# Kernel tuning notes

Measured on AMD Instinct MI355X. Metric: run time of the kernel, lower is better.

## Reference

```python
import jax, jax.numpy as jnp
import numpy as np

B, T, C = 2, 2048, 2048
N_HEAD = 16
HS = C // N_HEAD
D_LATENT = C // 2


def setup_inputs() -> dict:
    key = jax.random.key(0)
    ks = jax.random.split(key, 7)
    s = 0.02
    return {
        "x": jax.random.normal(ks[0], (B, T, C), dtype=jnp.float32),
        "Wq": jax.random.normal(ks[1], (C, C), dtype=jnp.float32) * s,
        "Wc": jax.random.normal(ks[2], (C, D_LATENT), dtype=jnp.float32) * s,
        "Wk": jax.random.normal(ks[3], (D_LATENT, C), dtype=jnp.float32) * s,
        "Wv": jax.random.normal(ks[4], (D_LATENT, C), dtype=jnp.float32) * s,
        "Wo": jax.random.normal(ks[5], (C, C), dtype=jnp.float32) * s,
        "bo": jnp.zeros((C,), dtype=jnp.float32),
    }


def reference(x, Wq, Wc, Wk, Wv, Wo, bo):
    b, t, c = x.shape
    # projections (torch Linear without bias, weights stored as (in, out))
    q = x @ Wq                    # (B,T,C)
    c_latent = x @ Wc             # (B,T,d_latent)
    k = c_latent @ Wk             # (B,T,C)
    v = c_latent @ Wv             # (B,T,C)
    # split heads -> (B,H,T,hs)
    q = q.reshape(b, t, N_HEAD, HS).transpose(0, 2, 1, 3)
    k = k.reshape(b, t, N_HEAD, HS).transpose(0, 2, 1, 3)
    v = v.reshape(b, t, N_HEAD, HS).transpose(0, 2, 1, 3)
    scale = 1.0 / jnp.sqrt(jnp.asarray(HS, dtype=x.dtype))
    scores = jnp.einsum('bhqd,bhkd->bhqk', q, k) * scale
    causal = jnp.tril(jnp.ones((t, t), dtype=bool))
    scores = jnp.where(causal, scores, jnp.finfo(scores.dtype).min)
    attn = jax.nn.softmax(scores, axis=-1)
    y = jnp.einsum('bhqk,bhkd->bhqd', attn, v)      # (B,H,T,hs)
    y = y.transpose(0, 2, 1, 3).reshape(b, t, c)
    return y @ Wo + bo
```

## Files before the change

### kernel.cpp

```cpp
#include <hip/hip_runtime.h>
#include <hip/hip_bf16.h>
#include <math.h>

typedef __hip_bfloat16 bf16;
typedef __attribute__((ext_vector_type(8))) short bf16x8;
typedef __attribute__((ext_vector_type(4))) float f32x4;

#define B_  2
#define T_  2048
#define C_  2048
#define H_  16
#define HS_ 128
#define DL_ 1024
#define M_  (B_ * T_)
#define NT64_ 32

__device__ inline void lds16(const bf16* g, bf16* l) {
    __builtin_amdgcn_global_load_lds(
        (const __attribute__((address_space(1))) void*)g,
        (__attribute__((address_space(3))) void*)l, 16, 0, 0);
}

__global__ __launch_bounds__(256) void cast_bf16_k(
    const float* __restrict__ in, bf16* __restrict__ out)
{
    const size_t i = ((size_t)blockIdx.x * 256 + threadIdx.x) * 8;
    const float4 a = *(const float4*)(in + i);
    const float4 b = *(const float4*)(in + i + 4);
    bf16 o[8];
    o[0] = __float2bfloat16(a.x); o[1] = __float2bfloat16(a.y);
    o[2] = __float2bfloat16(a.z); o[3] = __float2bfloat16(a.w);
    o[4] = __float2bfloat16(b.x); o[5] = __float2bfloat16(b.y);
    o[6] = __float2bfloat16(b.z); o[7] = __float2bfloat16(b.w);
    *(uint4*)(out + i) = *(const uint4*)o;
}

__global__ __launch_bounds__(256) void transpose_cast5(
    const float* __restrict__ s0, const float* __restrict__ s1,
    const float* __restrict__ s2, const float* __restrict__ s3,
    const float* __restrict__ s4,
    bf16* __restrict__ d0, bf16* __restrict__ d1, bf16* __restrict__ d2,
    bf16* __restrict__ d3, bf16* __restrict__ d4)
{
    const float* in; bf16* out; int R, Cc;
    switch (blockIdx.z) {
        case 0: in = s0; out = d0; R = C_;  Cc = C_;  break;
        case 1: in = s1; out = d1; R = C_;  Cc = DL_; break;
        case 2: in = s2; out = d2; R = DL_; Cc = C_;  break;
        case 3: in = s3; out = d3; R = DL_; Cc = C_;  break;
        default: in = s4; out = d4; R = C_; Cc = C_;  break;
    }
    const int bx = blockIdx.x * 32, by = blockIdx.y * 32;
    if (bx >= Cc || by >= R) return;
    __shared__ float t[32][33];
    const int tx = threadIdx.x & 31, ty = threadIdx.x >> 5;
#pragma unroll
    for (int i = 0; i < 32; i += 8)
        t[ty + i][tx] = in[(size_t)(by + ty + i) * Cc + bx + tx];
    __syncthreads();
#pragma unroll
    for (int i = 0; i < 32; i += 8)
        out[(size_t)(bx + ty + i) * R + by + tx] = __float2bfloat16(t[tx][ty + i]);
}

#define GEMM250_CORE(A_, Bt_, ldA_, ldB_, Kdim_)                               \
    __shared__ __align__(16) bf16 smem[3 * 24576];                 \
    const int tid  = threadIdx.x;                                              \
    const int lane = tid & 63;                                                 \
    const int wid  = tid >> 6;                                       \
    const int wr   = wid >> 1, wc = wid & 1;                    \
    const int quad = lane >> 4, l16 = lane & 15;                               \
    const int sw8  = (l16 >> 1) & 7;                                           \
    f32x4 acc[4][4];                                                           \
    _Pragma("unroll")                                                          \
    for (int i = 0; i < 4; i++)                                                \
        _Pragma("unroll")                                                      \
        for (int j = 0; j < 4; j++) acc[i][j] = (f32x4){0.f, 0.f, 0.f, 0.f};   \
    const int sr  = tid >> 3;                                       \
    const int ssl = ((tid & 7) ^ ((sr >> 1) & 7)) * 8;                         \
    const bf16* pa = (A_)  + (size_t)(m0 + sr) * (ldA_) + ssl;                 \
    const bf16* pb = (Bt_) + (size_t)(n0 + sr) * (ldB_) + ssl;                 \
    const size_t a64 = (size_t)64 * (ldA_), b64 = (size_t)64 * (ldB_);         \
    const int NT = (Kdim_) / 64;                                               \
    _Pragma("unroll")                                                          \
    for (int pt = 0; pt < 2; ++pt) {                  \
        bf16* dst = smem + pt * 24576 + tid * 8;                               \
        const size_t ko = (size_t)pt * 64;                                     \
        lds16(pa + ko,           dst);                                         \
        lds16(pa + a64 + ko,     dst + 4096);                                  \
        lds16(pa + 2*a64 + ko,   dst + 8192);                                  \
        lds16(pa + 3*a64 + ko,   dst + 12288);                                 \
        lds16(pb + ko,           dst + 16384);                                 \
        lds16(pb + b64 + ko,     dst + 20480);                                 \
    }                                                                          \
    int cur = 0, nxt2 = 2;                                                     \
    for (int t = 0; t < NT; ++t) {                                             \
        if (t == NT - 1) {                                                     \
            __asm__ __volatile__("s_waitcnt vmcnt(0)" ::: "memory");           \
        } else {                                                               \
            __asm__ __volatile__("s_waitcnt vmcnt(6)" ::: "memory");           \
        }                                                                      \
        __builtin_amdgcn_s_barrier();                                          \
        __builtin_amdgcn_sched_barrier(0);                                     \
        if (t + 2 < NT) {                                                      \
            bf16* dst = smem + nxt2 * 24576 + tid * 8;                         \
            const size_t ko = (size_t)(t + 2) * 64;                            \
            lds16(pa + ko,           dst);                                     \
            lds16(pa + a64 + ko,     dst + 4096);                              \
            lds16(pa + 2*a64 + ko,   dst + 8192);                              \
            lds16(pa + 3*a64 + ko,   dst + 12288);                             \
            lds16(pb + ko,           dst + 16384);                             \
            lds16(pb + b64 + ko,     dst + 20480);                             \
        }                                                                      \
        const bf16* Ab = smem + cur * 24576;                                   \
        const bf16* Bb = Ab + 16384;                                           \
        bf16x8 af[4][2], bfr[4][2];                                            \
        _Pragma("unroll")                                                      \
        for (int mi = 0; mi < 4; mi++)                                         \
            _Pragma("unroll")                                                  \
            for (int ks = 0; ks < 2; ks++)                                     \
                af[mi][ks] = *(const bf16x8*)&Ab[(wr*64 + mi*16 + l16)*64 +    \
                                                 (((ks<<2)|quad) ^ sw8)*8];    \
        _Pragma("unroll")                                                      \
        for (int ni = 0; ni < 4; ni++)                                         \
            _Pragma("unroll")                                                  \
            for (int ks = 0; ks < 2; ks++)                                     \
                bfr[ni][ks] = *(const bf16x8*)&Bb[(wc*64 + ni*16 + l16)*64 +   \
                                                  (((ks<<2)|quad) ^ sw8)*8];   \
        __builtin_amdgcn_s_setprio(1);                                         \
        _Pragma("unroll")                                                      \
        for (int ks = 0; ks < 2; ks++)                                         \
            _Pragma("unroll")                                                  \
            for (int mi = 0; mi < 4; mi++)                                     \
                _Pragma("unroll")                                              \
                for (int ni = 0; ni < 4; ni++)                                 \
                    acc[mi][ni] = __builtin_amdgcn_mfma_f32_16x16x32_bf16(     \
                        af[mi][ks], bfr[ni][ks], acc[mi][ni], 0, 0, 0);        \
        __builtin_amdgcn_s_setprio(0);                                         \
        cur  = (cur  == 2) ? 0 : cur  + 1;                                     \
        nxt2 = (nxt2 == 2) ? 0 : nxt2 + 1;                                     \
    }

__global__ __launch_bounds__(512, 2) void gemm_qc_250(
    const bf16* __restrict__ A, const bf16* __restrict__ Bt,
    bf16* __restrict__ Cq, bf16* __restrict__ Cc)
{
    const int m0 = blockIdx.y * 256, n0 = blockIdx.x * 128;
    GEMM250_CORE(A, Bt, C_, C_, C_)
    const bool is_q = (n0 < C_);
    const float scl = is_q ? 0.08838834764831845f : 1.0f;
    bf16* dst = is_q ? Cq : Cc;
    const int ld   = is_q ? C_ : DL_;
    const int coff = is_q ? 0 : C_;
#pragma unroll
    for (int mi = 0; mi < 4; mi++) {
#pragma unroll
        for (int ni = 0; ni < 4; ni++) {
            const int col = n0 - coff + wc * 64 + ni * 16 + l16;
#pragma unroll
            for (int r = 0; r < 4; r++) {
                const int row = m0 + wr * 64 + mi * 16 + quad * 4 + r;
                dst[(size_t)row * ld + col] = __float2bfloat16(acc[mi][ni][r] * scl);
            }
        }
    }
}

__global__ __launch_bounds__(512, 2) void gemm_kv_250(
    const bf16* __restrict__ clat, const bf16* __restrict__ Wk_t,
    const bf16* __restrict__ Wv_t, bf16* __restrict__ kk, bf16* __restrict__ vt)
{
    const int bid = blockIdx.x;
    const bf16 *A, *Bt; bf16* dst; int N, m0, n0;
    if (bid < 256) { A = clat; Bt = Wk_t; dst = kk; N = C_;
                     m0 = (bid >> 4) * 256; n0 = (bid & 15) * 128; }
    else           { const int t2 = bid - 256;
                     A = Wv_t; Bt = clat; dst = vt; N = M_;
                     m0 = (t2 >> 5) * 256; n0 = (t2 & 31) * 128; }
    GEMM250_CORE(A, Bt, DL_, DL_, DL_)
#pragma unroll
    for (int mi = 0; mi < 4; mi++) {
#pragma unroll
        for (int ni = 0; ni < 4; ni++) {
            const int col = n0 + wc * 64 + ni * 16 + l16;
#pragma unroll
            for (int r = 0; r < 4; r++) {
                const int row = m0 + wr * 64 + mi * 16 + quad * 4 + r;
                dst[(size_t)row * N + col] = __float2bfloat16(acc[mi][ni][r]);
            }
        }
    }
}

__global__ __launch_bounds__(512, 2) void gemm_out_250(
    const bf16* __restrict__ A, const bf16* __restrict__ Bt,
    float* __restrict__ Cf32, const float* __restrict__ bias)
{
    const int m0 = blockIdx.y * 256, n0 = blockIdx.x * 128;
    GEMM250_CORE(A, Bt, C_, C_, C_)
#pragma unroll
    for (int mi = 0; mi < 4; mi++) {
#pragma unroll
        for (int ni = 0; ni < 4; ni++) {
            const int col = n0 + wc * 64 + ni * 16 + l16;
#pragma unroll
            for (int r = 0; r < 4; r++) {
                const int row = m0 + wr * 64 + mi * 16 + quad * 4 + r;
                Cf32[(size_t)row * C_ + col] = acc[mi][ni][r] + bias[col];
            }
        }
    }
}

__global__ __launch_bounds__(256, 3) void flash_sb(
    const bf16* __restrict__ Q, const bf16* __restrict__ K,
    const bf16* __restrict__ Vt, bf16* __restrict__ Y)
{
    __shared__ __align__(16) bf16 Ks[4][64][32];
    __shared__ __align__(16) bf16 Vs[2][128][32];
    __shared__ __align__(16) bf16 Ps[4][16][72];
    const int tid  = threadIdx.x;
    const int lane = tid & 63, wv = tid >> 6;
    const int quad = lane >> 4, l16 = lane & 15;
    const int sw = (l16 >> 1) & 3;
    const int bid = blockIdx.x;
    const int bh = (bid & 7) * 4 + ((bid >> 3) & 3);
    const int pa = (NT64_ - 1) - (bid >> 5);
    const int b = bh >> 4, h = bh & 15;
    const int q0 = pa * 64;
    const int nj = pa + 1;
    const int rb = q0 + wv * 16;

    const int sr  = tid >> 2;
    const int ssl = ((tid & 3) ^ ((sr >> 1) & 3)) * 8;

    bf16x8 qf[4];
    {
        const size_t rQ = (size_t)(b * T_ + q0 + wv * 16 + l16) * C_ + h * HS_;
#pragma unroll
        for (int c = 0; c < 4; c++)
            qf[c] = *(const bf16x8*)(Q + rQ + c * 32 + quad * 8);
    }

    f32x4 o[8];
#pragma unroll
    for (int dt = 0; dt < 8; dt++) o[dt] = (f32x4){0.f, 0.f, 0.f, 0.f};
    float l_s[4] = {0.f, 0.f, 0.f, 0.f};

    auto stageK = [&](int j) {
        const int kv0 = j * 64;
#pragma unroll
        for (int kc = 0; kc < 4; kc++)
            lds16(K + (size_t)(b * T_ + kv0 + sr) * C_ + h * HS_ + kc * 32 + ssl,
                  &Ks[kc][0][0] + tid * 8);
    };
    auto stageV = [&](int j) {
        const int kv0 = j * 64;
#pragma unroll
        for (int vc = 0; vc < 2; vc++)
#pragma unroll
            for (int hf = 0; hf < 2; hf++)
                lds16(Vt + (size_t)(h * HS_ + hf * 64 + sr) * M_ + b * T_ + kv0 + vc * 32 + ssl,
                      &Vs[vc][hf * 64][0] + tid * 8);
    };

    auto sm_half = [&](const f32x4* s, int nt0, bool diag, int kv0) {
        float p[2][4];
#pragma unroll
        for (int t = 0; t < 2; t++)
#pragma unroll
            for (int r = 0; r < 4; r++) {
                const int nt = nt0 + t;
                float e = __expf(s[nt][r]);
                if (diag) {
                    const int col = kv0 + nt * 16 + l16;
                    const int row = rb + quad * 4 + r;
                    if (col > row) e = 0.f;
                }
                p[t][r] = e;
            }
#pragma unroll
        for (int r = 0; r < 4; r++) l_s[r] += p[0][r] + p[1][r];
#pragma unroll
        for (int t = 0; t < 2; t++)
#pragma unroll
            for (int r = 0; r < 4; r++)
                Ps[wv][quad * 4 + r][(nt0 + t) * 16 + l16] = __float2bfloat16(p[t][r]);
        return *(const bf16x8*)&Ps[wv][l16][nt0 * 16 + quad * 8];
    };

    stageK(0);
    stageV(0);
    for (int j = 0; j < nj; j++) {
        const int kv0 = j * 64;
        const bool more = (j + 1 < nj);

        __asm__ __volatile__("s_waitcnt vmcnt(4)" ::: "memory");
        __builtin_amdgcn_s_barrier();
        __builtin_amdgcn_sched_barrier(0);

        f32x4 s[4];
#pragma unroll
        for (int nt = 0; nt < 4; nt++) s[nt] = (f32x4){0.f, 0.f, 0.f, 0.f};
        __builtin_amdgcn_s_setprio(1);
#pragma unroll
        for (int c = 0; c < 4; c++) {
            bf16x8 kf[4];
#pragma unroll
            for (int nt = 0; nt < 4; nt++)
                kf[nt] = *(const bf16x8*)&Ks[c][nt * 16 + l16][(quad ^ sw) * 8];
#pragma unroll
            for (int nt = 0; nt < 4; nt++)
                s[nt] = __builtin_amdgcn_mfma_f32_16x16x32_bf16(qf[c], kf[nt], s[nt], 0, 0, 0);
        }
        __builtin_amdgcn_s_setprio(0);

        __asm__ __volatile__("s_waitcnt lgkmcnt(0)" ::: "memory");
        __builtin_amdgcn_s_barrier();
        __builtin_amdgcn_sched_barrier(0);
        if (more) stageK(j + 1);

        const bool dg = (j == nj - 1);
        const bf16x8 p0 = sm_half(s, 0, dg, kv0);
        const bf16x8 p1 = sm_half(s, 2, dg, kv0);

        if (more) {
            __asm__ __volatile__("s_waitcnt vmcnt(4)" ::: "memory");
        } else {
            __asm__ __volatile__("s_waitcnt vmcnt(0)" ::: "memory");
        }
        __builtin_amdgcn_s_barrier();
        __builtin_amdgcn_sched_barrier(0);

        __builtin_amdgcn_s_setprio(1);
#pragma unroll
        for (int dt = 0; dt < 8; dt++) {
            const bf16x8 vf0 = *(const bf16x8*)&Vs[0][dt * 16 + l16][(quad ^ sw) * 8];
            o[dt] = __builtin_amdgcn_mfma_f32_16x16x32_bf16(p0, vf0, o[dt], 0, 0, 0);
        }
#pragma unroll
        for (int dt = 0; dt < 8; dt++) {
            const bf16x8 vf1 = *(const bf16x8*)&Vs[1][dt * 16 + l16][(quad ^ sw) * 8];
            o[dt] = __builtin_amdgcn_mfma_f32_16x16x32_bf16(p1, vf1, o[dt], 0, 0, 0);
        }
        __builtin_amdgcn_s_setprio(0);

        __asm__ __volatile__("s_waitcnt lgkmcnt(0)" ::: "memory");
        __builtin_amdgcn_s_barrier();
        __builtin_amdgcn_sched_barrier(0);
        if (more) stageV(j + 1);
    }

    {
        float inv[4];
#pragma unroll
        for (int r = 0; r < 4; r++) {
            float l = l_s[r];
            l += __shfl_xor(l, 1);
            l += __shfl_xor(l, 2);
            l += __shfl_xor(l, 4);
            l += __shfl_xor(l, 8);
            inv[r] = 1.f / l;
        }
#pragma unroll
        for (int dt = 0; dt < 8; dt++)
#pragma unroll
            for (int r = 0; r < 4; r++)
                Y[(size_t)(b * T_ + rb + quad * 4 + r) * C_ + h * HS_ + dt * 16 + l16] =
                    __float2bfloat16(o[dt][r] * inv[r]);
    }
}

extern "C" void kernel_launch(void* const* d_in, const int* in_sizes, int n_in,
                              void* d_out, int out_size, void* d_ws, size_t ws_size,
                              hipStream_t stream) {
    const float* x  = (const float*)d_in[0];
    const float* Wq = (const float*)d_in[1];
    const float* Wc = (const float*)d_in[2];
    const float* Wk = (const float*)d_in[3];
    const float* Wv = (const float*)d_in[4];
    const float* Wo = (const float*)d_in[5];
    const float* bo = (const float*)d_in[6];
    float* out = (float*)d_out;

    bf16* ws   = (bf16*)d_ws;
    bf16* x_bf = ws;
    bf16* Wq_t = x_bf + (size_t)M_ * C_;
    bf16* Wc_t = Wq_t + (size_t)C_ * C_;
    bf16* Wk_t = Wc_t + (size_t)DL_ * C_;
    bf16* Wv_t = Wk_t + (size_t)C_ * DL_;
    bf16* Wo_t = Wv_t + (size_t)C_ * DL_;
    bf16* q    = Wo_t + (size_t)C_ * C_;
    bf16* clat = q    + (size_t)M_ * C_;
    bf16* kk   = clat + (size_t)M_ * DL_;
    bf16* vt   = kk   + (size_t)M_ * C_;
    bf16* y    = vt   + (size_t)C_ * M_;

    const dim3 blk(256);
    const dim3 blk512(512);

    cast_bf16_k<<<dim3((M_ * C_) / (256 * 8)), blk, 0, stream>>>(x, x_bf);
    transpose_cast5<<<dim3(C_ / 32, C_ / 32, 5), blk, 0, stream>>>(
        Wq, Wc, Wk, Wv, Wo, Wq_t, Wc_t, Wk_t, Wv_t, Wo_t);

    gemm_qc_250<<<dim3((C_ + DL_) / 128, M_ / 256), blk512, 0, stream>>>(
        x_bf, Wq_t, q, clat);
    gemm_kv_250<<<dim3(512), blk512, 0, stream>>>(clat, Wk_t, Wv_t, kk, vt);

    flash_sb<<<dim3(NT64_ * H_ * B_), blk, 0, stream>>>(q, kk, vt, y);

    gemm_out_250<<<dim3(C_ / 128, M_ / 256), blk512, 0, stream>>>(
        y, Wo_t, out, bo);
}
```

Before: 329.1 us.

## Replace QC and KV GEMMs with 256x256 tile ping-pong kernel using phased MFMA

```diff
diff --git a/kernel.cpp b/kernel.cpp
--- a/kernel.cpp
+++ b/kernel.cpp
@@ -61,6 +61,150 @@
 #pragma unroll
     for (int i = 0; i < 32; i += 8)
         out[(size_t)(bx + ty + i) * R + by + tx] = __float2bfloat16(t[tx][ty + i]);
+}
+
+#define STAGE_AQ(qq, ko, bb)                                                   \
+    lds16(pa + (size_t)(qq) * 64 * (size_t)ldA + (ko),                         \
+          &As[bb][0][0] + (qq) * 4096 + tid * 8);
+#define STAGE_BQ(qq, ko, bb)                                                   \
+    lds16(pb + (size_t)(qq) * 64 * (size_t)ldB + (ko),                         \
+          &Bs[bb][0][0] + (qq) * 4096 + tid * 8);
+
+#define PHASE8(qm_, qn_)                                                       \
+    {                                                                          \
+        bf16x8 af[4][2], bfr[2][2];                                            \
+        _Pragma("unroll")                                                      \
+        for (int mi = 0; mi < 4; mi++)                                         \
+            _Pragma("unroll")                                                  \
+            for (int ks = 0; ks < 2; ks++)                                     \
+                af[mi][ks] = *(const bf16x8*)&Abase[((qm_)*64 + mi*16 + l16)*64\
+                                     + (((ks<<2)|quad) ^ sw8)*8];              \
+        _Pragma("unroll")                                                      \
+        for (int ni = 0; ni < 2; ni++)                                         \
+            _Pragma("unroll")                                                  \
+            for (int ks = 0; ks < 2; ks++)                                     \
+                bfr[ni][ks] = *(const bf16x8*)&Bbase[((qn_)*32 + ni*16 + l16)*64\
+                                     + (((ks<<2)|quad) ^ sw8)*8];              \
+        __builtin_amdgcn_s_barrier();                                          \
+        __asm__ __volatile__("s_waitcnt lgkmcnt(0)" ::: "memory");             \
+        __builtin_amdgcn_sched_barrier(0);                                     \
+        __builtin_amdgcn_s_setprio(1);                                         \
+        _Pragma("unroll")                                                      \
+        for (int ks = 0; ks < 2; ks++)                                         \
+            _Pragma("unroll")                                                  \
+            for (int mi = 0; mi < 4; mi++)                                     \
+                _Pragma("unroll")                                              \
+                for (int ni = 0; ni < 2; ni++)                                 \
+                    acc[(qm_)*4 + mi][(qn_)*2 + ni] =                          \
+                        __builtin_amdgcn_mfma_f32_16x16x32_bf16(               \
+                            af[mi][ks], bfr[ni][ks],                           \
+                            acc[(qm_)*4 + mi][(qn_)*2 + ni], 0, 0, 0);         \
+        __builtin_amdgcn_s_setprio(0);                                         \
+        __builtin_amdgcn_s_barrier();                                          \
+    }
+
+#define GEMM8P_CORE(A_, Bt_, ldA_, ldB_, Kdim_)                                \
+    __shared__ __align__(16) bf16 As[2][256][64];                   \
+    __shared__ __align__(16) bf16 Bs[2][256][64];                   \
+    const int tid  = threadIdx.x;                                              \
+    const int lane = tid & 63;                                                 \
+    const int wid  = tid >> 6;                                       \
+    const int wm   = wid >> 2, wn = wid & 3;                      \
+    const int quad = lane >> 4, l16 = lane & 15;                               \
+    const int sw8  = (l16 >> 1) & 7;                                           \
+    const int ldA = (ldA_), ldB = (ldB_);                                      \
+    f32x4 acc[8][4];                                                           \
+    _Pragma("unroll")                                                          \
+    for (int i = 0; i < 8; i++)                                                \
+        _Pragma("unroll")                                                      \
+        for (int j = 0; j < 4; j++) acc[i][j] = (f32x4){0.f, 0.f, 0.f, 0.f};   \
+    const int sr  = tid >> 3;                            \
+    const int ssl = ((tid & 7) ^ ((sr >> 1) & 7)) * 8;                         \
+    const bf16* pa = (A_)  + (size_t)(m0 + sr) * ldA + ssl;                    \
+    const bf16* pb = (Bt_) + (size_t)(n0 + sr) * ldB + ssl;                    \
+    const int NT = (Kdim_) / 64;                                               \
+    _Pragma("unroll")                                                          \
+    for (int pt = 0; pt < 2; ++pt) {                  \
+        const size_t ko = (size_t)pt * 64;                                     \
+        STAGE_AQ(0, ko, pt) STAGE_AQ(1, ko, pt)                                \
+        STAGE_AQ(2, ko, pt) STAGE_AQ(3, ko, pt)                                \
+        STAGE_BQ(0, ko, pt) STAGE_BQ(1, ko, pt)                                \
+        STAGE_BQ(2, ko, pt) STAGE_BQ(3, ko, pt)                                \
+    }                                                                          \
+    for (int t = 0; t < NT; ++t) {                                             \
+        const int buf = t & 1;                                                 \
+        if (t == NT - 1) {                                                     \
+            __asm__ __volatile__("s_waitcnt vmcnt(0)" ::: "memory");           \
+        } else {                                                               \
+            __asm__ __volatile__("s_waitcnt vmcnt(8)" ::: "memory");           \
+        }                                                                      \
+        __builtin_amdgcn_s_barrier();                      \
+        __builtin_amdgcn_sched_barrier(0);                                     \
+        const bf16* Abase = &As[buf][wm * 128][0];                             \
+        const bf16* Bbase = &Bs[buf][wn * 64][0];                              \
+        const bool pf = (t + 2 < NT);                                          \
+        const size_t ko2 = (size_t)(t + 2) * 64;                               \
+        PHASE8(0, 0)                                                           \
+        PHASE8(0, 1)                                                           \
+        if (pf) { STAGE_AQ(0, ko2, buf) STAGE_AQ(2, ko2, buf) }                \
+        PHASE8(1, 0)                                                           \
+        PHASE8(1, 1)                                                           \
+        if (pf) {                                                              \
+            STAGE_AQ(1, ko2, buf) STAGE_AQ(3, ko2, buf)                        \
+            STAGE_BQ(0, ko2, buf) STAGE_BQ(1, ko2, buf)                        \
+            STAGE_BQ(2, ko2, buf) STAGE_BQ(3, ko2, buf)                        \
+        }                                                                      \
+    }
+
+__global__ __launch_bounds__(512, 2) void gemm_qc_8p(
+    const bf16* __restrict__ A, const bf16* __restrict__ Bt,
+    bf16* __restrict__ Cq, bf16* __restrict__ Cc)
+{
+    const int m0 = blockIdx.y * 256, n0 = blockIdx.x * 256;
+    GEMM8P_CORE(A, Bt, C_, C_, C_)
+    const bool is_q = (n0 < C_);
+    const float scl = is_q ? 0.08838834764831845f : 1.0f;
+    bf16* dst = is_q ? Cq : Cc;
+    const int ld   = is_q ? C_ : DL_;
+    const int coff = is_q ? 0 : C_;
+#pragma unroll
+    for (int mig = 0; mig < 8; mig++) {
+#pragma unroll
+        for (int nig = 0; nig < 4; nig++) {
+            const int col = n0 - coff + wn * 64 + nig * 16 + l16;
+#pragma unroll
+            for (int r = 0; r < 4; r++) {
+                const int row = m0 + wm * 128 + mig * 16 + quad * 4 + r;
+                dst[(size_t)row * ld + col] = __float2bfloat16(acc[mig][nig][r] * scl);
+            }
+        }
+    }
+}
+
+__global__ __launch_bounds__(512, 2) void gemm_kv_8p(
+    const bf16* __restrict__ clat, const bf16* __restrict__ Wk_t,
+    const bf16* __restrict__ Wv_t, bf16* __restrict__ kk, bf16* __restrict__ vt)
+{
+    const int bid = blockIdx.x;
+    const bf16 *A, *Bt; bf16* dst; int N, m0, n0;
+    if (bid < 128) { A = clat; Bt = Wk_t; dst = kk; N = C_;
+                     m0 = (bid >> 3) * 256; n0 = (bid & 7) * 256; }
+    else           { const int t2 = bid - 128;
+                     A = Wv_t; Bt = clat; dst = vt; N = M_;
+                     m0 = (t2 >> 4) * 256; n0 = (t2 & 15) * 256; }
+    GEMM8P_CORE(A, Bt, DL_, DL_, DL_)
+#pragma unroll
+    for (int mig = 0; mig < 8; mig++) {
+#pragma unroll
+        for (int nig = 0; nig < 4; nig++) {
+            const int col = n0 + wn * 64 + nig * 16 + l16;
+#pragma unroll
+            for (int r = 0; r < 4; r++) {
+                const int row = m0 + wm * 128 + mig * 16 + quad * 4 + r;
+                dst[(size_t)row * N + col] = __float2bfloat16(acc[mig][nig][r]);
+            }
+        }
+    }
 }
 
 #define GEMM250_CORE(A_, Bt_, ldA_, ldB_, Kdim_)                               \
@@ -141,57 +285,6 @@
         nxt2 = (nxt2 == 2) ? 0 : nxt2 + 1;                                     \
     }
 
-__global__ __launch_bounds__(512, 2) void gemm_qc_250(
-    const bf16* __restrict__ A, const bf16* __restrict__ Bt,
-    bf16* __restrict__ Cq, bf16* __restrict__ Cc)
-{
-    const int m0 = blockIdx.y * 256, n0 = blockIdx.x * 128;
-    GEMM250_CORE(A, Bt, C_, C_, C_)
-    const bool is_q = (n0 < C_);
-    const float scl = is_q ? 0.08838834764831845f : 1.0f;
-    bf16* dst = is_q ? Cq : Cc;
-    const int ld   = is_q ? C_ : DL_;
-    const int coff = is_q ? 0 : C_;
-#pragma unroll
-    for (int mi = 0; mi < 4; mi++) {
-#pragma unroll
-        for (int ni = 0; ni < 4; ni++) {
-            const int col = n0 - coff + wc * 64 + ni * 16 + l16;
-#pragma unroll
-            for (int r = 0; r < 4; r++) {
-                const int row = m0 + wr * 64 + mi * 16 + quad * 4 + r;
-                dst[(size_t)row * ld + col] = __float2bfloat16(acc[mi][ni][r] * scl);
-            }
-        }
-    }
-}
-
-__global__ __launch_bounds__(512, 2) void gemm_kv_250(
-    const bf16* __restrict__ clat, const bf16* __restrict__ Wk_t,
-    const bf16* __restrict__ Wv_t, bf16* __restrict__ kk, bf16* __restrict__ vt)
-{
-    const int bid = blockIdx.x;
-    const bf16 *A, *Bt; bf16* dst; int N, m0, n0;
-    if (bid < 256) { A = clat; Bt = Wk_t; dst = kk; N = C_;
-                     m0 = (bid >> 4) * 256; n0 = (bid & 15) * 128; }
-    else           { const int t2 = bid - 256;
-                     A = Wv_t; Bt = clat; dst = vt; N = M_;
-                     m0 = (t2 >> 5) * 256; n0 = (t2 & 31) * 128; }
-    GEMM250_CORE(A, Bt, DL_, DL_, DL_)
-#pragma unroll
-    for (int mi = 0; mi < 4; mi++) {
-#pragma unroll
-        for (int ni = 0; ni < 4; ni++) {
-            const int col = n0 + wc * 64 + ni * 16 + l16;
-#pragma unroll
-            for (int r = 0; r < 4; r++) {
-                const int row = m0 + wr * 64 + mi * 16 + quad * 4 + r;
-                dst[(size_t)row * N + col] = __float2bfloat16(acc[mi][ni][r]);
-            }
-        }
-    }
-}
-
 __global__ __launch_bounds__(512, 2) void gemm_out_250(
     const bf16* __restrict__ A, const bf16* __restrict__ Bt,
     float* __restrict__ Cf32, const float* __restrict__ bias)
@@ -403,9 +496,9 @@
     transpose_cast5<<<dim3(C_ / 32, C_ / 32, 5), blk, 0, stream>>>(
         Wq, Wc, Wk, Wv, Wo, Wq_t, Wc_t, Wk_t, Wv_t, Wo_t);
 
-    gemm_qc_250<<<dim3((C_ + DL_) / 128, M_ / 256), blk512, 0, stream>>>(
+    gemm_qc_8p<<<dim3((C_ + DL_) / 256, M_ / 256), blk512, 0, stream>>>(
         x_bf, Wq_t, q, clat);
-    gemm_kv_250<<<dim3(512), blk512, 0, stream>>>(clat, Wk_t, Wv_t, kk, vt);
+    gemm_kv_8p<<<dim3(256), blk512, 0, stream>>>(clat, Wk_t, Wv_t, kk, vt);
 
     flash_sb<<<dim3(NT64_ * H_ * B_), blk, 0, stream>>>(q, kk, vt, y);
 
```

Measured after the change: 374.5 us. 1.14x slower.
